# Optimization experiments

Measured on AMD Instinct MI355X. Metric: run time of the kernel, lower is better.

Reference implementation:

```python
import jax, jax.numpy as jnp
import numpy as np

B, T, P, D, H = 4, 12, 196, 512, 8
DH = D // H
EPS = 1e-6


def _norm(x, alpha, bias):
    # torch Norm: alpha*(x-mean)/(std_unbiased+eps)+bias, std uses Bessel correction (ddof=1)
    mu = jnp.mean(x, axis=-1, keepdims=True)
    sd = jnp.std(x, axis=-1, ddof=1, keepdims=True)
    return alpha * (x - mu) / (sd + EPS) + bias


def setup_inputs() -> dict:
    key = jax.random.key(0)
    ks = jax.random.split(key, 12)
    s = 0.02

    def n(k, shape, scale=s):
        return jax.random.normal(k, shape, jnp.float32) * scale

    return {
        "x": jax.random.normal(ks[0], (B, T, P, D), jnp.float32),
        "Wq": n(ks[1], (D, D)), "bq": jnp.zeros((D,), jnp.float32),
        "Wk": n(ks[2], (D, D)), "bk": jnp.zeros((D,), jnp.float32),
        "Wv": n(ks[3], (D, D)), "bv": jnp.zeros((D,), jnp.float32),
        "in_a": jnp.ones((D,), jnp.float32), "in_b": jnp.zeros((D,), jnp.float32),
        "attn_a": jnp.ones((D,), jnp.float32), "attn_b": jnp.zeros((D,), jnp.float32),
        "out_a": jnp.ones((D,), jnp.float32), "out_b": jnp.zeros((D,), jnp.float32),
        "Wt": n(ks[4], (T, D, D)), "bt": jnp.zeros((T, D), jnp.float32),
        "pos": n(ks[5], (T, T, P, D), 0.02),
        "W1": n(ks[6], (2 * D, D)), "b1": jnp.zeros((2 * D,), jnp.float32),
        "W2": n(ks[7], (D, 2 * D)), "b2": jnp.zeros((D,), jnp.float32),
    }


def reference(x, Wq, bq, Wk, bk, Wv, bv, in_a, in_b, attn_a, attn_b,
              out_a, out_b, Wt, bt, pos, W1, b1, W2, b2):
    x2 = _norm(x, in_a, in_b)

    def proj(W, b):
        # [B,T,P,D] -> [B,T,H,P,DH]
        return (x2 @ W.T + b).reshape(B, T, P, H, DH).transpose(0, 1, 3, 2, 4)

    Q = proj(Wq, bq)
    K = proj(Wk, bk)
    V = proj(Wv, bv)

    # all-pairs temporal cross attention: [B,t,u,H,Pq,Pk]
    qk = jnp.einsum('btijk,builk->btuijl', Q, K) / np.sqrt(DH)
    attn = jax.nn.softmax(qk, axis=-1)  # no mask, dropout=0
    av = jnp.einsum('btuijl,builk->btuijk', attn, V)  # [B,t,u,H,P,DH]
    av = av.transpose(0, 1, 2, 4, 3, 5).reshape(B, T, T, P, D)
    av = _norm(av, attn_a, attn_b)
    x2p = av + pos  # pos broadcasts over batch

    # per-u Linear fused as one batched contraction, summed over u
    tc = jnp.einsum('btupd,ued->btpe', x2p / T, Wt) + jnp.sum(bt, axis=0)
    x = x + jax.nn.gelu(tc, approximate=False)

    x2 = _norm(x, out_a, out_b)
    h = jax.nn.gelu(x2 @ W1.T + b1, approximate=False)
    y = jax.nn.gelu(h @ W2.T + b2, approximate=False)
    return x + y
```

## Files before the change

### kernel.cpp

```cpp
#include <hip/hip_runtime.h>
#include <hip/hip_bf16.h>

typedef __hip_bfloat16 bf16;

typedef __bf16 bfrag8 __attribute__((ext_vector_type(8)));
typedef __bf16 bfrag4 __attribute__((ext_vector_type(4)));
typedef float  ffrag4 __attribute__((ext_vector_type(4)));
typedef float  ffrag16 __attribute__((ext_vector_type(16)));

#define EPS 1e-6f

__device__ __forceinline__ float gelu_exact(float v) {
  return 0.5f * v * (1.0f + erff(v * 0.7071067811865475f));
}

__device__ __forceinline__ void async16(const void* g, void* s) {
  __builtin_amdgcn_global_load_lds(
      (const __attribute__((address_space(1))) unsigned int*)g,
      (__attribute__((address_space(3))) unsigned int*)s, 16, 0, 0);
}

struct alignas(16) bf16x8 { bf16 v[8]; };
struct alignas(4)  bf16p2 { __bf16 v[2]; };

__global__ __launch_bounds__(256) void conv_w_kernel(
    const float* __restrict__ Wq, const float* __restrict__ Wk,
    const float* __restrict__ Wv, const float* __restrict__ W1,
    const float* __restrict__ W2, const float* __restrict__ Wt,
    __bf16* __restrict__ dst)
{
  size_t e = ((size_t)blockIdx.x * 256 + threadIdx.x) * 8;
  const float* src; size_t off;
  if      (e <  262144) { src = Wq; off = e; }
  else if (e <  524288) { src = Wk; off = e -  262144; }
  else if (e <  786432) { src = Wv; off = e -  524288; }
  else if (e < 1310720) { src = W1; off = e -  786432; }
  else if (e < 1835008) { src = W2; off = e - 1310720; }
  else if (e < 4980736) { src = Wt; off = e - 1835008; }
  else return;
  float4 f0 = *(const float4*)(src + off);
  float4 f1 = *(const float4*)(src + off + 4);
  bfrag8 o;
  o[0] = (__bf16)f0.x; o[1] = (__bf16)f0.y; o[2] = (__bf16)f0.z; o[3] = (__bf16)f0.w;
  o[4] = (__bf16)f1.x; o[5] = (__bf16)f1.y; o[6] = (__bf16)f1.z; o[7] = (__bf16)f1.w;
  *(bfrag8*)(dst + e) = o;
}

__global__ __launch_bounds__(512) void sum_bt_kernel(
    const float* __restrict__ bt, float* __restrict__ sbt)
{
  int n = threadIdx.x;
  float s = 0.f;
#pragma unroll
  for (int u = 0; u < 12; ++u) s += bt[u * 512 + n];
  sbt[n] = s;
}

__global__ __launch_bounds__(64) void norm_f32_to_bf16_kernel(
    const float* __restrict__ in, __bf16* __restrict__ out,
    const float* __restrict__ alpha, const float* __restrict__ beta)
{
  size_t row = blockIdx.x;
  int l = threadIdx.x;
  const float* r = in + row * 512 + l * 8;
  float4 v0 = *(const float4*)(r);
  float4 v1 = *(const float4*)(r + 4);
  float f[8] = {v0.x, v0.y, v0.z, v0.w, v1.x, v1.y, v1.z, v1.w};
  float s = 0.f, ss = 0.f;
#pragma unroll
  for (int q = 0; q < 8; ++q) { s += f[q]; ss += f[q] * f[q]; }
#pragma unroll
  for (int off = 32; off; off >>= 1) { s += __shfl_xor(s, off); ss += __shfl_xor(ss, off); }
  float mu = s * (1.f / 512.f);
  float var = fmaxf((ss - 512.f * mu * mu) * (1.f / 511.f), 0.f);
  float inv = 1.f / (sqrtf(var) + EPS);
  const float* al = alpha + l * 8;
  const float* be = beta + l * 8;
  float4 a0 = *(const float4*)al, a1 = *(const float4*)(al + 4);
  float4 b0 = *(const float4*)be, b1 = *(const float4*)(be + 4);
  float aa[8] = {a0.x, a0.y, a0.z, a0.w, a1.x, a1.y, a1.z, a1.w};
  float bb[8] = {b0.x, b0.y, b0.z, b0.w, b1.x, b1.y, b1.z, b1.w};
  bfrag8 o;
#pragma unroll
  for (int q = 0; q < 8; ++q) o[q] = (__bf16)(aa[q] * (f[q] - mu) * inv + bb[q]);
  *(bfrag8*)(out + row * 512 + l * 8) = o;
}

__global__ __launch_bounds__(64) void norm_av_kernel(
    bf16* __restrict__ av, const float* __restrict__ alpha,
    const float* __restrict__ beta, const float* __restrict__ pos)
{
  size_t row = blockIdx.x;
  int l = threadIdx.x;
  bf16* r = av + row * 512 + (size_t)l * 8;
  bf16x8 ib = *(const bf16x8*)r;
  float f[8];
#pragma unroll
  for (int q = 0; q < 8; ++q) f[q] = __bfloat162float(ib.v[q]);
  float s = 0.f, ss = 0.f;
#pragma unroll
  for (int q = 0; q < 8; ++q) { s += f[q]; ss += f[q] * f[q]; }
#pragma unroll
  for (int off = 32; off; off >>= 1) { s += __shfl_xor(s, off); ss += __shfl_xor(ss, off); }
  float mu = s * (1.f / 512.f);
  float var = fmaxf((ss - 512.f * mu * mu) * (1.f / 511.f), 0.f);
  float inv = 1.f / (sqrtf(var) + EPS);
  size_t prow = row % 28224;
  const float* pr = pos + prow * 512 + l * 8;
  float4 p0 = *(const float4*)pr, p1 = *(const float4*)(pr + 4);
  const float* al = alpha + l * 8;
  const float* be = beta + l * 8;
  float4 a0 = *(const float4*)al, a1 = *(const float4*)(al + 4);
  float4 b0 = *(const float4*)be, b1 = *(const float4*)(be + 4);
  float pa[8] = {p0.x, p0.y, p0.z, p0.w, p1.x, p1.y, p1.z, p1.w};
  float aa[8] = {a0.x, a0.y, a0.z, a0.w, a1.x, a1.y, a1.z, a1.w};
  float bb[8] = {b0.x, b0.y, b0.z, b0.w, b1.x, b1.y, b1.z, b1.w};
  bf16x8 ob;
#pragma unroll
  for (int q = 0; q < 8; ++q)
    ob.v[q] = __float2bfloat16(aa[q] * (f[q] - mu) * inv + bb[q] + pa[q]);
  *(bf16x8*)r = ob;
}

__global__ __launch_bounds__(256) void mfma_nt_kernel(
    const __bf16* __restrict__ A,
    const __bf16* __restrict__ Bq, const __bf16* __restrict__ Bk,
    const __bf16* __restrict__ Bv,
    const float* __restrict__ bq, const float* __restrict__ bk,
    const float* __restrict__ bv,
    __bf16* __restrict__ oq, __bf16* __restrict__ ok, __bf16* __restrict__ ov,
    const float* __restrict__ res, float* __restrict__ fout,
    int K, int mode)
{
  __shared__ __bf16 As[128 * 32];
  __shared__ __bf16 Bs[128 * 32];
  int tid = threadIdx.x;
  int m0 = blockIdx.y * 128;
  int n0g = blockIdx.x * 128;

  const __bf16* Bsel; const float* biassel; __bf16* osel; int ncol0;
  if (mode == 0) {
    int sel = n0g >> 9;
    Bsel = sel == 0 ? Bq : (sel == 1 ? Bk : Bv);
    biassel = sel == 0 ? bq : (sel == 1 ? bk : bv);
    osel = sel == 0 ? oq : (sel == 1 ? ok : ov);
    ncol0 = n0g & 511;
  } else {
    Bsel = Bq; biassel = bq; osel = oq; ncol0 = n0g;
  }

  int srow = tid >> 2, scol = (tid & 3) * 8;
  int r0 = m0 + srow;      if (r0 > 9407) r0 = 9407;
  int r1 = m0 + 64 + srow; if (r1 > 9407) r1 = 9407;
  const __bf16* a0 = A + (size_t)r0 * K + scol;
  const __bf16* a1 = A + (size_t)r1 * K + scol;
  const __bf16* b0 = Bsel + (size_t)(ncol0 + srow) * K + scol;
  const __bf16* b1 = Bsel + (size_t)(ncol0 + 64 + srow) * K + scol;
  char* sa0 = (char*)As + tid * 16;
  char* sa1 = (char*)As + 4096 + tid * 16;
  char* sb0 = (char*)Bs + tid * 16;
  char* sb1 = (char*)Bs + 4096 + tid * 16;

  int l = tid & 63, w = tid >> 6;
  int lm = l & 15, lq = l >> 4;
  int wm = w >> 1, wn = w & 1;

  ffrag4 acc[4][4] = {};
  for (int k0 = 0; k0 < K; k0 += 32) {
    __syncthreads();
    async16(a0 + k0, sa0);
    async16(a1 + k0, sa1);
    async16(b0 + k0, sb0);
    async16(b1 + k0, sb1);
    __syncthreads();
    bfrag8 af[4], bfr[4];
#pragma unroll
    for (int i = 0; i < 4; ++i)
      af[i] = *(const bfrag8*)&As[(wm * 64 + i * 16 + lm) * 32 + lq * 8];
#pragma unroll
    for (int j = 0; j < 4; ++j)
      bfr[j] = *(const bfrag8*)&Bs[(wn * 64 + j * 16 + lm) * 32 + lq * 8];
#pragma unroll
    for (int i = 0; i < 4; ++i)
#pragma unroll
      for (int j = 0; j < 4; ++j)
        acc[i][j] = __builtin_amdgcn_mfma_f32_16x16x32_bf16(af[i], bfr[j], acc[i][j], 0, 0, 0);
  }

#pragma unroll
  for (int i = 0; i < 4; ++i) {
    int mbase = m0 + wm * 64 + i * 16 + lq * 4;
#pragma unroll
    for (int j = 0; j < 4; ++j) {
      int n = ncol0 + wn * 64 + j * 16 + lm;
      float bj = biassel[n];
#pragma unroll
      for (int r = 0; r < 4; ++r) {
        int mr = mbase + r;
        if (mr < 9408) {
          float v = acc[i][j][r] + bj;
          if (mode == 0)      osel[(size_t)mr * 512 + n] = (__bf16)v;
          else if (mode == 1) osel[(size_t)mr * 1024 + n] = (__bf16)gelu_exact(v);
          else                fout[(size_t)mr * 512 + n] =
                                res[(size_t)mr * 512 + n] + gelu_exact(v);
        }
      }
    }
  }
}

__global__ __launch_bounds__(256) void mfma_tc_kernel(
    const __bf16* __restrict__ X2p, const __bf16* __restrict__ Wtb,
    const float* __restrict__ sbt, const float* __restrict__ xin,
    float* __restrict__ xmid)
{
  __shared__ __bf16 As[64 * 32];
  __shared__ __bf16 Bs[128 * 32];
  int tid = threadIdx.x;
  int m0 = blockIdx.y * 64;
  int n0 = blockIdx.x * 128;

  int srow = tid >> 2, scol = (tid & 3) * 8;
  int r0 = m0 + srow;
  int btq0 = r0 / 196, p0 = r0 - btq0 * 196;
  const __bf16* a0 = X2p + (size_t)btq0 * 1204224 + (size_t)p0 * 512 + scol;
  const __bf16* b0 = Wtb + (size_t)(n0 + srow) * 512 + scol;
  const __bf16* b1 = Wtb + (size_t)(n0 + 64 + srow) * 512 + scol;
  char* sa0 = (char*)As + tid * 16;
  char* sb0 = (char*)Bs + tid * 16;
  char* sb1 = (char*)Bs + 4096 + tid * 16;

  int l = tid & 63, w = tid >> 6;
  int lm = l & 15, lq = l >> 4;
  int wm = w >> 1, wn = w & 1;

  ffrag4 acc[2][4] = {};
  for (int u = 0; u < 12; ++u) {
    size_t au = (size_t)u * 100352;
    size_t bu = (size_t)u * 262144;
    for (int d0 = 0; d0 < 512; d0 += 32) {
      __syncthreads();
      async16(a0 + au + d0, sa0);
      async16(b0 + bu + d0, sb0);
      async16(b1 + bu + d0, sb1);
      __syncthreads();
      bfrag8 af[2], bfr[4];
#pragma unroll
      for (int i = 0; i < 2; ++i)
        af[i] = *(const bfrag8*)&As[(wm * 32 + i * 16 + lm) * 32 + lq * 8];
#pragma unroll
      for (int j = 0; j < 4; ++j)
        bfr[j] = *(const bfrag8*)&Bs[(wn * 64 + j * 16 + lm) * 32 + lq * 8];
#pragma unroll
      for (int i = 0; i < 2; ++i)
#pragma unroll
        for (int j = 0; j < 4; ++j)
          acc[i][j] = __builtin_amdgcn_mfma_f32_16x16x32_bf16(af[i], bfr[j], acc[i][j], 0, 0, 0);
    }
  }

#pragma unroll
  for (int i = 0; i < 2; ++i) {
    int mbase = m0 + wm * 32 + i * 16 + lq * 4;
#pragma unroll
    for (int j = 0; j < 4; ++j) {
      int n = n0 + wn * 64 + j * 16 + lm;
      float bj = sbt[n];
#pragma unroll
      for (int r = 0; r < 4; ++r) {
        int mr = mbase + r;
        float v = acc[i][j][r] * (1.f / 12.f) + bj;
        xmid[(size_t)mr * 512 + n] = xin[(size_t)mr * 512 + n] + gelu_exact(v);
      }
    }
  }
}

__global__ __launch_bounds__(512, 4) void attn_kernel(
    const __bf16* __restrict__ Q, const __bf16* __restrict__ K,
    const __bf16* __restrict__ V, __bf16* __restrict__ av)
{
  __shared__ __bf16 Ks[196 * 64];
  __shared__ __bf16 Vt[64 * 208];
  __shared__ __bf16 Pball[8 * 32 * 20];

  int bid = blockIdx.x;
  int half = bid & 1;
  int h = (bid >> 1) & 7;
  int r0 = bid >> 4;
  int u = r0 % 12;
  int b = r0 / 12;

  const __bf16* Kp = K + ((size_t)(b * 12 + u) * 196) * 512 + h * 64;
  const __bf16* Vp = V + ((size_t)(b * 12 + u) * 196) * 512 + h * 64;

  for (int idx = threadIdx.x; idx < 196 * 8; idx += 512) {
    int r = idx >> 3, g = idx & 7;
    *(bfrag8*)&Ks[r * 64 + ((g ^ (r & 7)) * 8)] =
        *(const bfrag8*)&Kp[(size_t)r * 512 + g * 8];
  }
  for (int idx = threadIdx.x; idx < 64 * 6; idx += 512) {
    int r = idx / 6, c2 = 196 + (idx % 6) * 2;
    bf16p2 z; z.v[0] = (__bf16)0.f; z.v[1] = (__bf16)0.f;
    *(bf16p2*)&Vt[r * 208 + c2] = z;
  }
  for (int idx = threadIdx.x; idx < 98 * 8; idx += 512) {
    int r2 = (idx % 98) * 2, c8 = (idx / 98) * 8;
    bfrag8 va = *(const bfrag8*)&Vp[(size_t)r2 * 512 + c8];
    bfrag8 vb = *(const bfrag8*)&Vp[(size_t)(r2 + 1) * 512 + c8];
#pragma unroll
    for (int e = 0; e < 8; ++e) {
      bf16p2 pr; pr.v[0] = va[e]; pr.v[1] = vb[e];
      *(bf16p2*)&Vt[(c8 + e) * 208 + r2] = pr;
    }
  }
  __syncthreads();

  int w = threadIdx.x >> 6, l = threadIdx.x & 63;
  int l5 = l >> 5, c = l & 31;
  __bf16* Pb = Pball + w * (32 * 20);

  for (int unit = w; unit < 42; unit += 8) {
    int t = unit / 7, qt = unit - t * 7;
    int tq = half * 6 + t;
    const __bf16* Qp = Q + ((size_t)(b * 12 + tq) * 196) * 512 + h * 64;
    __bf16* avp = av + ((size_t)((b * 12 + tq) * 12 + u) * 196) * 512 + h * 64;
    int q0 = qt * 32;

    const __bf16* qp = Qp + (size_t)(q0 + c) * 512 + l5 * 8;
    bfrag8 qf[4];
    qf[0] = *(const bfrag8*)(qp);
    qf[1] = *(const bfrag8*)(qp + 16);
    qf[2] = *(const bfrag8*)(qp + 32);
    qf[3] = *(const bfrag8*)(qp + 48);

    ffrag16 O0, O1;
#pragma unroll
    for (int g = 0; g < 16; ++g) { O0[g] = 0.f; O1[g] = 0.f; }
    float sumacc = 0.f;

    for (int nt = 0; nt < 7; ++nt) {
      int key = nt * 32 + c; if (key > 195) key = 195;
      const __bf16* kbase = &Ks[key * 64];
      int kx = key & 7;

      ffrag16 s;
#pragma unroll
      for (int g = 0; g < 16; ++g) s[g] = 0.f;
#pragma unroll
      for (int kc = 0; kc < 4; ++kc) {
        bfrag8 kf = *(const bfrag8*)&kbase[(((kc * 2 + l5) ^ kx) * 8)];
        s = __builtin_amdgcn_mfma_f32_32x32x16_bf16(kf, qf[kc], s, 0, 0, 0);
      }

#pragma unroll
      for (int g = 0; g < 16; ++g) {
        float e = __expf(s[g] * 0.125f);
        bool keep = (nt < 6) || ((g < 4) && (l5 == 0));
        e = keep ? e : 0.f;
        s[g] = e;
        sumacc += e;
      }

#pragma unroll
      for (int sub = 0; sub < 2; ++sub) {
        if (nt == 6 && sub == 1) break;
#pragma unroll
        for (int g = 0; g < 8; ++g) {
          int gg = sub * 8 + g;
          int k16 = (gg & 3) + 8 * ((gg >> 2) & 1) + 4 * l5;
          Pb[c * 20 + k16] = (__bf16)s[gg];
        }
        __threadfence_block();
        int ch = nt * 2 + sub;
        bfrag4 plo = *(const bfrag4*)&Pb[c * 20 + l5 * 8];
        bfrag4 phi = *(const bfrag4*)&Pb[c * 20 + l5 * 8 + 4];
        bfrag8 pa = __builtin_shufflevector(plo, phi, 0, 1, 2, 3, 4, 5, 6, 7);
        bfrag8 v0 = *(const bfrag8*)&Vt[(size_t)(c     ) * 208 + ch * 16 + l5 * 8];
        bfrag8 v1 = *(const bfrag8*)&Vt[(size_t)(c + 32) * 208 + ch * 16 + l5 * 8];
        O0 = __builtin_amdgcn_mfma_f32_32x32x16_bf16(pa, v0, O0, 0, 0, 0);
        O1 = __builtin_amdgcn_mfma_f32_32x32x16_bf16(pa, v1, O1, 0, 0, 0);
      }
    }

    float stot = sumacc + __shfl_xor(sumacc, 32);

#pragma unroll
    for (int g = 0; g < 16; ++g) {
      int row = (g & 3) + 8 * (g >> 2) + 4 * l5;
      float sq = __shfl(stot, row);
      float iv = __builtin_amdgcn_rcpf(sq);
      int q = q0 + row;
      if (q < 196) {
        size_t base = (size_t)q * 512 + c;
        avp[base]      = (__bf16)(O0[g] * iv);
        avp[base + 32] = (__bf16)(O1[g] * iv);
      }
    }
  }
}

extern "C" void kernel_launch(void* const* d_in, const int* in_sizes, int n_in,
                              void* d_out, int out_size, void* d_ws, size_t ws_size,
                              hipStream_t stream)
{
  const float* x      = (const float*)d_in[0];
  const float* Wq     = (const float*)d_in[1];
  const float* bq     = (const float*)d_in[2];
  const float* Wk     = (const float*)d_in[3];
  const float* bk     = (const float*)d_in[4];
  const float* Wv     = (const float*)d_in[5];
  const float* bv     = (const float*)d_in[6];
  const float* in_a   = (const float*)d_in[7];
  const float* in_b   = (const float*)d_in[8];
  const float* attn_a = (const float*)d_in[9];
  const float* attn_b = (const float*)d_in[10];
  const float* out_a  = (const float*)d_in[11];
  const float* out_b  = (const float*)d_in[12];
  const float* Wt     = (const float*)d_in[13];
  const float* bt     = (const float*)d_in[14];
  const float* pos    = (const float*)d_in[15];
  const float* W1     = (const float*)d_in[16];
  const float* b1     = (const float*)d_in[17];
  const float* W2     = (const float*)d_in[18];
  const float* b2     = (const float*)d_in[19];

  char* ws = (char*)d_ws;
  const size_t bfb = (size_t)9408 * 512 * 2;
  __bf16* x2b  = (__bf16*)(ws);
  __bf16* Qb   = (__bf16*)(ws + bfb);
  __bf16* Kb   = (__bf16*)(ws + 2 * bfb);
  __bf16* Vb   = (__bf16*)(ws + 3 * bfb);
  __bf16* av   = (__bf16*)(ws + 4 * bfb);
  char*   wreg = ws + 4 * bfb + (size_t)115605504;
  __bf16* Wqb  = (__bf16*)(wreg);
  __bf16* Wkb  = (__bf16*)(wreg) + 262144;
  __bf16* Wvb  = (__bf16*)(wreg) + 524288;
  __bf16* W1b  = (__bf16*)(wreg) + 786432;
  __bf16* W2b  = (__bf16*)(wreg) + 1310720;
  __bf16* Wtb  = (__bf16*)(wreg) + 1835008;
  float*  sbt  = (float*)(wreg + 9961472);
  float*  xmid = (float*)(ws);
  __bf16* x3b  = (__bf16*)(ws + 2 * bfb);
  __bf16* hb   = (__bf16*)(ws + 4 * bfb);
  float*  out  = (float*)d_out;

  conv_w_kernel<<<2432, 256, 0, stream>>>(Wq, Wk, Wv, W1, W2, Wt, (__bf16*)wreg);
  sum_bt_kernel<<<1, 512, 0, stream>>>(bt, sbt);
  norm_f32_to_bf16_kernel<<<9408, 64, 0, stream>>>(x, x2b, in_a, in_b);
  mfma_nt_kernel<<<dim3(12, 74), 256, 0, stream>>>(
      x2b, Wqb, Wkb, Wvb, bq, bk, bv, Qb, Kb, Vb, nullptr, nullptr, 512, 0);
  attn_kernel<<<768, 512, 0, stream>>>(Qb, Kb, Vb, av);
  norm_av_kernel<<<112896, 64, 0, stream>>>((bf16*)av, attn_a, attn_b, pos);
  mfma_tc_kernel<<<dim3(4, 147), 256, 0, stream>>>(av, Wtb, sbt, x, xmid);
  norm_f32_to_bf16_kernel<<<9408, 64, 0, stream>>>(xmid, x3b, out_a, out_b);
  mfma_nt_kernel<<<dim3(8, 74), 256, 0, stream>>>(
      x3b, W1b, nullptr, nullptr, b1, nullptr, nullptr, hb, nullptr, nullptr,
      nullptr, nullptr, 512, 1);
  mfma_nt_kernel<<<dim3(4, 74), 256, 0, stream>>>(
      hb, W2b, nullptr, nullptr, b2, nullptr, nullptr, nullptr, nullptr, nullptr,
      xmid, out, 1024, 2);
}
```

Before: 541.4 us.

## Split-K temporal GEMM over u with atomics, fuse epilogue with norm, shrink GEMM tiles

The temporal-combine GEMM is split across four groups of three u slices with a z grid dimension. Partial sums are accumulated into a zeroed fp32 buffer with atomicAdd. A new per-row kernel applies the bias, GELU and residual and fuses the following output norm, which replaces the separate norm launch. The generic NT GEMM drops from 128-row to 64-row tiles, which doubles the block count for better CU occupancy. The cost is extra atomic traffic, a zeroing pass, and less B-tile reuse per block.

```diff
diff --git a/kernel.cpp b/kernel.cpp
--- a/kernel.cpp
+++ b/kernel.cpp
@@ -22,6 +22,11 @@
 
 struct alignas(16) bf16x8 { bf16 v[8]; };
 struct alignas(4)  bf16p2 { __bf16 v[2]; };
+
+__global__ __launch_bounds__(256) void zero_acc_kernel(float* __restrict__ p) {
+  size_t i = ((size_t)blockIdx.x * 256 + threadIdx.x) * 4;
+  *(float4*)(p + i) = make_float4(0.f, 0.f, 0.f, 0.f);
+}
 
 __global__ __launch_bounds__(256) void conv_w_kernel(
     const float* __restrict__ Wq, const float* __restrict__ Wk,
@@ -132,10 +137,10 @@
     const float* __restrict__ res, float* __restrict__ fout,
     int K, int mode)
 {
-  __shared__ __bf16 As[128 * 32];
+  __shared__ __bf16 As[64 * 32];
   __shared__ __bf16 Bs[128 * 32];
   int tid = threadIdx.x;
-  int m0 = blockIdx.y * 128;
+  int m0 = blockIdx.y * 64;
   int n0g = blockIdx.x * 128;
 
   const __bf16* Bsel; const float* biassel; __bf16* osel; int ncol0;
@@ -150,14 +155,10 @@
   }
 
   int srow = tid >> 2, scol = (tid & 3) * 8;
-  int r0 = m0 + srow;      if (r0 > 9407) r0 = 9407;
-  int r1 = m0 + 64 + srow; if (r1 > 9407) r1 = 9407;
-  const __bf16* a0 = A + (size_t)r0 * K + scol;
-  const __bf16* a1 = A + (size_t)r1 * K + scol;
+  const __bf16* a0 = A + (size_t)(m0 + srow) * K + scol;
   const __bf16* b0 = Bsel + (size_t)(ncol0 + srow) * K + scol;
   const __bf16* b1 = Bsel + (size_t)(ncol0 + 64 + srow) * K + scol;
   char* sa0 = (char*)As + tid * 16;
-  char* sa1 = (char*)As + 4096 + tid * 16;
   char* sb0 = (char*)Bs + tid * 16;
   char* sb1 = (char*)Bs + 4096 + tid * 16;
 
@@ -165,31 +166,30 @@
   int lm = l & 15, lq = l >> 4;
   int wm = w >> 1, wn = w & 1;
 
-  ffrag4 acc[4][4] = {};
+  ffrag4 acc[2][4] = {};
   for (int k0 = 0; k0 < K; k0 += 32) {
     __syncthreads();
     async16(a0 + k0, sa0);
-    async16(a1 + k0, sa1);
     async16(b0 + k0, sb0);
     async16(b1 + k0, sb1);
     __syncthreads();
-    bfrag8 af[4], bfr[4];
-#pragma unroll
-    for (int i = 0; i < 4; ++i)
-      af[i] = *(const bfrag8*)&As[(wm * 64 + i * 16 + lm) * 32 + lq * 8];
+    bfrag8 af[2], bfr[4];
+#pragma unroll
+    for (int i = 0; i < 2; ++i)
+      af[i] = *(const bfrag8*)&As[(wm * 32 + i * 16 + lm) * 32 + lq * 8];
 #pragma unroll
     for (int j = 0; j < 4; ++j)
       bfr[j] = *(const bfrag8*)&Bs[(wn * 64 + j * 16 + lm) * 32 + lq * 8];
 #pragma unroll
-    for (int i = 0; i < 4; ++i)
+    for (int i = 0; i < 2; ++i)
 #pragma unroll
       for (int j = 0; j < 4; ++j)
         acc[i][j] = __builtin_amdgcn_mfma_f32_16x16x32_bf16(af[i], bfr[j], acc[i][j], 0, 0, 0);
   }
 
 #pragma unroll
-  for (int i = 0; i < 4; ++i) {
-    int mbase = m0 + wm * 64 + i * 16 + lq * 4;
+  for (int i = 0; i < 2; ++i) {
+    int mbase = m0 + wm * 32 + i * 16 + lq * 4;
 #pragma unroll
     for (int j = 0; j < 4; ++j) {
       int n = ncol0 + wn * 64 + j * 16 + lm;
@@ -197,13 +197,11 @@
 #pragma unroll
       for (int r = 0; r < 4; ++r) {
         int mr = mbase + r;
-        if (mr < 9408) {
-          float v = acc[i][j][r] + bj;
-          if (mode == 0)      osel[(size_t)mr * 512 + n] = (__bf16)v;
-          else if (mode == 1) osel[(size_t)mr * 1024 + n] = (__bf16)gelu_exact(v);
-          else                fout[(size_t)mr * 512 + n] =
-                                res[(size_t)mr * 512 + n] + gelu_exact(v);
-        }
+        float v = acc[i][j][r] + bj;
+        if (mode == 0)      osel[(size_t)mr * 512 + n] = (__bf16)v;
+        else if (mode == 1) osel[(size_t)mr * 1024 + n] = (__bf16)gelu_exact(v);
+        else                fout[(size_t)mr * 512 + n] =
+                              res[(size_t)mr * 512 + n] + gelu_exact(v);
       }
     }
   }
@@ -211,14 +209,14 @@
 
 __global__ __launch_bounds__(256) void mfma_tc_kernel(
     const __bf16* __restrict__ X2p, const __bf16* __restrict__ Wtb,
-    const float* __restrict__ sbt, const float* __restrict__ xin,
-    float* __restrict__ xmid)
+    float* __restrict__ accb)
 {
   __shared__ __bf16 As[64 * 32];
   __shared__ __bf16 Bs[128 * 32];
   int tid = threadIdx.x;
   int m0 = blockIdx.y * 64;
   int n0 = blockIdx.x * 128;
+  int ug = blockIdx.z * 3;
 
   int srow = tid >> 2, scol = (tid & 3) * 8;
   int r0 = m0 + srow;
@@ -235,7 +233,7 @@
   int wm = w >> 1, wn = w & 1;
 
   ffrag4 acc[2][4] = {};
-  for (int u = 0; u < 12; ++u) {
+  for (int u = ug; u < ug + 3; ++u) {
     size_t au = (size_t)u * 100352;
     size_t bu = (size_t)u * 262144;
     for (int d0 = 0; d0 < 512; d0 += 32) {
@@ -265,15 +263,57 @@
 #pragma unroll
     for (int j = 0; j < 4; ++j) {
       int n = n0 + wn * 64 + j * 16 + lm;
-      float bj = sbt[n];
 #pragma unroll
       for (int r = 0; r < 4; ++r) {
         int mr = mbase + r;
-        float v = acc[i][j][r] * (1.f / 12.f) + bj;
-        xmid[(size_t)mr * 512 + n] = xin[(size_t)mr * 512 + n] + gelu_exact(v);
+        atomicAdd(accb + (size_t)mr * 512 + n, acc[i][j][r]);
       }
     }
   }
+}
+
+__global__ __launch_bounds__(64) void tc_epi_norm_kernel(
+    const float* __restrict__ accb, const float* __restrict__ x,
+    const float* __restrict__ sbt,
+    const float* __restrict__ alpha, const float* __restrict__ beta,
+    float* __restrict__ xmid, __bf16* __restrict__ x3b)
+{
+  size_t row = blockIdx.x;
+  int l = threadIdx.x;
+  size_t base = row * 512 + l * 8;
+  float4 c0 = *(const float4*)(accb + base);
+  float4 c1 = *(const float4*)(accb + base + 4);
+  float4 x0 = *(const float4*)(x + base);
+  float4 x1 = *(const float4*)(x + base + 4);
+  float4 s0 = *(const float4*)(sbt + l * 8);
+  float4 s1 = *(const float4*)(sbt + l * 8 + 4);
+  float cc[8] = {c0.x, c0.y, c0.z, c0.w, c1.x, c1.y, c1.z, c1.w};
+  float xx[8] = {x0.x, x0.y, x0.z, x0.w, x1.x, x1.y, x1.z, x1.w};
+  float sv[8] = {s0.x, s0.y, s0.z, s0.w, s1.x, s1.y, s1.z, s1.w};
+  float f[8];
+#pragma unroll
+  for (int q = 0; q < 8; ++q)
+    f[q] = xx[q] + gelu_exact(cc[q] * (1.f / 12.f) + sv[q]);
+  *(float4*)(xmid + base)     = make_float4(f[0], f[1], f[2], f[3]);
+  *(float4*)(xmid + base + 4) = make_float4(f[4], f[5], f[6], f[7]);
+  float s = 0.f, ss = 0.f;
+#pragma unroll
+  for (int q = 0; q < 8; ++q) { s += f[q]; ss += f[q] * f[q]; }
+#pragma unroll
+  for (int off = 32; off; off >>= 1) { s += __shfl_xor(s, off); ss += __shfl_xor(ss, off); }
+  float mu = s * (1.f / 512.f);
+  float var = fmaxf((ss - 512.f * mu * mu) * (1.f / 511.f), 0.f);
+  float inv = 1.f / (sqrtf(var) + EPS);
+  const float* al = alpha + l * 8;
+  const float* be = beta + l * 8;
+  float4 a0 = *(const float4*)al, a1 = *(const float4*)(al + 4);
+  float4 b0 = *(const float4*)be, b1 = *(const float4*)(be + 4);
+  float aa[8] = {a0.x, a0.y, a0.z, a0.w, a1.x, a1.y, a1.z, a1.w};
+  float bb[8] = {b0.x, b0.y, b0.z, b0.w, b1.x, b1.y, b1.z, b1.w};
+  bfrag8 o;
+#pragma unroll
+  for (int q = 0; q < 8; ++q) o[q] = (__bf16)(aa[q] * (f[q] - mu) * inv + bb[q]);
+  *(bfrag8*)(x3b + base) = o;
 }
 
 __global__ __launch_bounds__(512, 4) void attn_kernel(
@@ -440,6 +480,7 @@
   __bf16* W2b  = (__bf16*)(wreg) + 1310720;
   __bf16* Wtb  = (__bf16*)(wreg) + 1835008;
   float*  sbt  = (float*)(wreg + 9961472);
+  float*  accb = (float*)(wreg + 9963520);
   float*  xmid = (float*)(ws);
   __bf16* x3b  = (__bf16*)(ws + 2 * bfb);
   __bf16* hb   = (__bf16*)(ws + 4 * bfb);
@@ -447,17 +488,18 @@
 
   conv_w_kernel<<<2432, 256, 0, stream>>>(Wq, Wk, Wv, W1, W2, Wt, (__bf16*)wreg);
   sum_bt_kernel<<<1, 512, 0, stream>>>(bt, sbt);
+  zero_acc_kernel<<<4704, 256, 0, stream>>>(accb);
   norm_f32_to_bf16_kernel<<<9408, 64, 0, stream>>>(x, x2b, in_a, in_b);
-  mfma_nt_kernel<<<dim3(12, 74), 256, 0, stream>>>(
+  mfma_nt_kernel<<<dim3(12, 147), 256, 0, stream>>>(
       x2b, Wqb, Wkb, Wvb, bq, bk, bv, Qb, Kb, Vb, nullptr, nullptr, 512, 0);
   attn_kernel<<<768, 512, 0, stream>>>(Qb, Kb, Vb, av);
   norm_av_kernel<<<112896, 64, 0, stream>>>((bf16*)av, attn_a, attn_b, pos);
-  mfma_tc_kernel<<<dim3(4, 147), 256, 0, stream>>>(av, Wtb, sbt, x, xmid);
-  norm_f32_to_bf16_kernel<<<9408, 64, 0, stream>>>(xmid, x3b, out_a, out_b);
-  mfma_nt_kernel<<<dim3(8, 74), 256, 0, stream>>>(
+  mfma_tc_kernel<<<dim3(4, 147, 4), 256, 0, stream>>>(av, Wtb, accb);
+  tc_epi_norm_kernel<<<9408, 64, 0, stream>>>(accb, x, sbt, out_a, out_b, xmid, x3b);
+  mfma_nt_kernel<<<dim3(8, 147), 256, 0, stream>>>(
       x3b, W1b, nullptr, nullptr, b1, nullptr, nullptr, hb, nullptr, nullptr,
       nullptr, nullptr, 512, 1);
-  mfma_nt_kernel<<<dim3(4, 74), 256, 0, stream>>>(
+  mfma_nt_kernel<<<dim3(4, 147), 256, 0, stream>>>(
       hb, W2b, nullptr, nullptr, b2, nullptr, nullptr, nullptr, nullptr, nullptr,
       xmid, out, 1024, 2);
 }
```

After: 529.8 us. -2.2%, faster.
